# Performance work log

Hardware: AMD Instinct MI355X
Metric: run time of the kernel (lower is better)

The kernel has to match this reference:

```python
import jax, jax.numpy as jnp
import numpy as np

N_SLOTS = 65536
KEY_DIM = 64
VAL_DIM = 64
N_QUERIES = 8192
TOPK = 4
LR = 1e-3
MOMENTUM = 0.9
WD = 1e-4


def setup_inputs() -> dict:
    key = jax.random.key(0)
    k1, k2, k3, k4 = jax.random.split(key, 4)
    return {
        "queries": jax.random.normal(k1, (N_QUERIES, KEY_DIM), jnp.float32),
        "grads": jax.random.normal(k2, (N_QUERIES, TOPK, VAL_DIM), jnp.float32) * 0.05,
        "keys": jax.random.normal(k3, (N_SLOTS, KEY_DIM), jnp.float32) * 0.02,
        "vals": jax.random.normal(k4, (N_SLOTS, VAL_DIM), jnp.float32) * 0.02,
        "mom_vals": jnp.zeros((N_SLOTS, VAL_DIM), jnp.float32),
        "topk": TOPK,
    }


def reference(queries, grads, keys, vals, mom_vals, topk):
    # --- retrieve_topk ---
    sim = queries @ keys.T                      # [N, n_slots]
    _, idx = jax.lax.top_k(sim, topk)           # [N, topk] int32
    retrieved = vals[idx]                       # [N, topk, val_dim]

    # --- inner_update (no_grad in original) ---
    n_slots, val_dim = vals.shape
    idx_flat = idx.reshape(-1)                  # [N*topk]
    grads_flat = grads.reshape(-1, val_dim)     # [N*topk, val_dim]
    slot_grads = jax.ops.segment_sum(grads_flat, idx_flat, num_segments=n_slots)
    counts = jax.ops.segment_sum(
        jnp.ones_like(idx_flat, dtype=jnp.float32), idx_flat, num_segments=n_slots
    )
    mask = counts > 0
    # average grads per touched slot; untouched slots stay zero
    slot_grads = jnp.where(mask[:, None], slot_grads / jnp.maximum(counts, 1.0)[:, None], slot_grads)

    new_mom = MOMENTUM * mom_vals + slot_grads
    update_delta = -LR * (new_mom + WD * vals)
    final_update = jnp.where(mask[:, None], update_delta, 0.0)
    new_vals = vals + final_update
    return retrieved, idx, new_vals, new_mom
```

## Files before the change

kernel.cpp:

```cpp
#include <hip/hip_runtime.h>
#include <stdint.h>

#define N_SLOTS   65536
#define KEY_DIM   64
#define VAL_DIM   64
#define N_QUERIES 8192
#define TOPK      4
#define LR        1e-3f
#define MOMENTUM  0.9f
#define WD        1e-4f

#define NCHUNK 16
#define CHUNK  (N_SLOTS / NCHUNK)
#define TILE_SLOTS 128
#define TILES_PER_CHUNK (CHUNK / TILE_SLOTS)
#define SUBT 8
#define QPB 128

#define ZF4   ((N_SLOTS * VAL_DIM + N_SLOTS) / 4)
#define ZBLK  (ZF4 / 256)
#define QBLK  (N_QUERIES * 8 / 256)
#define KBLK  (N_SLOTS * 8 / 256)

typedef __attribute__((ext_vector_type(8))) _Float16 f16x8;
typedef __attribute__((ext_vector_type(2))) __fp16   fp16x2;
typedef __attribute__((ext_vector_type(4))) float    f32x4;
union F16 { uint4 u; f16x8 h; };
union PK  { fp16x2 h2; uint32_t u; };

__device__ __forceinline__ uint32_t pk2(float a, float b) {
    PK p; p.h2 = __builtin_amdgcn_cvt_pkrtz(a, b); return p.u;
}

__device__ __forceinline__ uint32_t med3u(uint32_t a, uint32_t b, uint32_t c) {
    uint32_t d;
    asm("v_med3_u32 %0, %1, %2, %3" : "=v"(d) : "v"(a), "v"(b), "v"(c));
    return d;
}

__device__ __forceinline__ uint64_t ord64(double d) {
    uint64_t u = (uint64_t)__double_as_longlong(d);
    return (u & 0x8000000000000000ull) ? ~u : (u | 0x8000000000000000ull);
}
__device__ __forceinline__ void ins4(uint64_t* t, uint64_t key) {
    if (key > t[3]) {
        t[3] = key;
        if (t[3] > t[2]) { uint64_t x = t[2]; t[2] = t[3]; t[3] = x; }
        if (t[2] > t[1]) { uint64_t x = t[1]; t[1] = t[2]; t[2] = x; }
        if (t[1] > t[0]) { uint64_t x = t[0]; t[0] = t[1]; t[1] = x; }
    }
}
__device__ __forceinline__ void cswap64(uint64_t& x, uint64_t& y) {
    uint64_t hi = x > y ? x : y;
    uint64_t lo = x > y ? y : x;
    x = hi; y = lo;
}
__device__ __forceinline__ void merge4_64(uint64_t* a, uint64_t b0, uint64_t b1,
                                          uint64_t b2, uint64_t b3) {
    uint64_t m0 = a[0] > b3 ? a[0] : b3;
    uint64_t m1 = a[1] > b2 ? a[1] : b2;
    uint64_t m2 = a[2] > b1 ? a[2] : b1;
    uint64_t m3 = a[3] > b0 ? a[3] : b0;
    cswap64(m0, m2); cswap64(m1, m3); cswap64(m0, m1); cswap64(m2, m3);
    a[0] = m0; a[1] = m1; a[2] = m2; a[3] = m3;
}
__device__ __forceinline__ void cswap32(uint32_t& x, uint32_t& y) {
    uint32_t hi = max(x, y);
    uint32_t lo = min(x, y);
    x = hi; y = lo;
}
__device__ __forceinline__ void merge4_32(uint32_t* a, uint32_t b0, uint32_t b1,
                                          uint32_t b2, uint32_t b3) {
    uint32_t m0 = max(a[0], b3);
    uint32_t m1 = max(a[1], b2);
    uint32_t m2 = max(a[2], b1);
    uint32_t m3 = max(a[3], b0);
    cswap32(m0, m2); cswap32(m1, m3); cswap32(m0, m1); cswap32(m2, m3);
    a[0] = m0; a[1] = m1; a[2] = m2; a[3] = m3;
}

__device__ __forceinline__ void gload16(const void* g, void* l) {
    __builtin_amdgcn_global_load_lds(
        (const __attribute__((address_space(1))) uint32_t*)g,
        (__attribute__((address_space(3))) uint32_t*)l, 16, 0, 0);
}

__global__ void kA_pack(const float* __restrict__ queries,
                        const float* __restrict__ keys,
                        uint4* __restrict__ qpack, uint4* __restrict__ kpack,
                        float4* __restrict__ zbuf) {
    const int b = blockIdx.x, tid = threadIdx.x;
    if (b < ZBLK) {
        zbuf[b * 256 + tid] = (float4){0.f, 0.f, 0.f, 0.f};
    } else if (b < ZBLK + QBLK) {
        int e = (b - ZBLK) * 256 + tid;
        const float4* src = (const float4*)(queries + (size_t)e * 8);
        float4 a = src[0], v = src[1];
        uint4 u;
        u.x = pk2(a.x, a.y); u.y = pk2(a.z, a.w);
        u.z = pk2(v.x, v.y); u.w = pk2(v.z, v.w);
        qpack[e] = u;
    } else {
        int e = (b - ZBLK - QBLK) * 256 + tid;
        int slot = e >> 3, k8 = e & 7;
        const float4* src = (const float4*)(keys + (size_t)slot * KEY_DIM + k8 * 8);
        float4 a = src[0], v = src[1];
        uint4 u;
        u.x = pk2(a.x, a.y); u.y = pk2(a.z, a.w);
        u.z = pk2(v.x, v.y); u.w = pk2(v.z, v.w);
        int tile = slot >> 7, r = slot & 127;
        kpack[(size_t)tile * 1024 + r * 8 + (k8 ^ (r & 7))] = u;
    }
}

__global__ __launch_bounds__(256, 4) void k1_screen(
        const uint4* __restrict__ qpack, const uint4* __restrict__ kpack,
        uint32_t* __restrict__ cand) {
    __shared__ uint4 sbuf[2048];

    const int tid = threadIdx.x;
    const int w = tid >> 6, lane = tid & 63;
    const int lcol = lane & 15, lrow = lane >> 4;
    const int chunk  = blockIdx.x;
    const int qblock = blockIdx.y;

    f16x8 B[2][2];
    #pragma unroll
    for (int j = 0; j < 2; ++j) {
        #pragma unroll
        for (int ks = 0; ks < 2; ++ks) {
            int q = qblock * QPB + w * 32 + j * 16 + lcol;
            F16 t; t.u = qpack[q * 8 + lrow + ks * 4];
            B[j][ks] = t.h;
        }
    }

    uint32_t kk[2][4] = {{0u,0u,0u,0u},{0u,0u,0u,0u}};

    const uint4* gbase = kpack + (size_t)(chunk * TILES_PER_CHUNK) * 1024;
    const int x0 = lrow ^ (lcol & 7);
    const int base_b = lcol * 128 + x0 * 16;
    const f32x4 zacc = {4.0f, 4.0f, 4.0f, 4.0f};

#define STAGE(tt, bb) do {                                                    \
        const uint4* gg = gbase + (size_t)(tt) * 1024 + w * 256 + lane;       \
        char* ldst = (char*)sbuf + (bb) * 16384 + w * 4096;                   \
        _Pragma("unroll")                                                     \
        for (int i_ = 0; i_ < 4; ++i_)                                        \
            gload16((const void*)(gg + i_ * 64), (void*)(ldst + i_ * 1024));  \
    } while (0)

    STAGE(0, 0);

    #pragma unroll 1
    for (int t = 0; t < TILES_PER_CHUNK; ++t) {
        __syncthreads();
        if (t < TILES_PER_CHUNK - 1) STAGE(t + 1, (t + 1) & 1);
        const char* sbb = (const char*)sbuf + (t & 1) * 16384;
        const uint32_t tbase = (uint32_t)(t * 32) + (uint32_t)lrow;

        #pragma unroll
        for (int sub = 0; sub < SUBT; ++sub) {
            uint4 ua0 = *(const uint4*)(sbb + base_b + sub * 2048);
            uint4 ua1 = *(const uint4*)(sbb + (base_b ^ 64) + sub * 2048);
            F16 a0, a1; a0.u = ua0; a1.u = ua1;
            const uint32_t idb = tbase + (uint32_t)(sub * 4);

            #pragma unroll
            for (int j = 0; j < 2; ++j) {
                f32x4 acc = __builtin_amdgcn_mfma_f32_16x16x32_f16(a0.h, B[j][0], zacc, 0, 0, 0);
                acc = __builtin_amdgcn_mfma_f32_16x16x32_f16(a1.h, B[j][1], acc, 0, 0, 0);
                float m = fmaxf(fmaxf(fmaxf(acc[0], acc[1]), acc[2]), acc[3]);
                uint32_t key = (__float_as_uint(m) & 0xFFFFFC00u) | idb;
                uint32_t t0 = kk[j][0], t1 = kk[j][1], t2 = kk[j][2], t3 = kk[j][3];
                kk[j][0] = max(t0, key);
                kk[j][1] = med3u(t0, t1, key);
                kk[j][2] = med3u(t1, t2, key);
                kk[j][3] = med3u(t2, t3, key);
            }
        }
    }
#undef STAGE

    #pragma unroll
    for (int j = 0; j < 2; ++j) {
        uint32_t s4[4] = {kk[j][0], kk[j][1], kk[j][2], kk[j][3]};
        #pragma unroll
        for (int m = 16; m <= 32; m <<= 1) {
            uint32_t b0 = (uint32_t)__shfl_xor((int)s4[0], m, 64);
            uint32_t b1 = (uint32_t)__shfl_xor((int)s4[1], m, 64);
            uint32_t b2 = (uint32_t)__shfl_xor((int)s4[2], m, 64);
            uint32_t b3 = (uint32_t)__shfl_xor((int)s4[3], m, 64);
            merge4_32(s4, b0, b1, b2, b3);
        }
        if (lane < 16) {
            int q = qblock * QPB + w * 32 + j * 16 + lane;
            uint4 c;
            c.x = s4[0] & 1023u; c.y = s4[1] & 1023u;
            c.z = s4[2] & 1023u; c.w = s4[3] & 1023u;
            *(uint4*)&cand[((size_t)q * NCHUNK + chunk) * 4] = c;
        }
    }
}

__global__ __launch_bounds__(256) void k2_rescore(
        const uint32_t* __restrict__ cand,
        const float* __restrict__ queries, const float* __restrict__ keys,
        const float* __restrict__ vals, const float* __restrict__ grads,
        float* __restrict__ retrieved, float* __restrict__ idx_f,
        float* __restrict__ slot_grads, float* __restrict__ counts) {
    int w = threadIdx.x >> 6, lane = threadIdx.x & 63;
    int q = blockIdx.x * 4 + w;
    int seg = lane & 3;

    const float4* qp = (const float4*)(queries + (size_t)q * KEY_DIM);
    float4 q0 = qp[seg * 4 + 0], q1 = qp[seg * 4 + 1];
    float4 q2 = qp[seg * 4 + 2], q3 = qp[seg * 4 + 3];
    const uint32_t* cq = cand + (size_t)q * 64;

    uint64_t s4[4] = {0ull, 0ull, 0ull, 0ull};
    #pragma unroll 4
    for (int it = 0; it < 16; ++it) {
        int r = it * 16 + (lane >> 2);
        uint32_t grow = cq[r >> 2];
        int slot = (r >> 4) * CHUNK + (int)(grow >> 2) * 16
                 + (int)(grow & 3) * 4 + (r & 3);
        const float4* kp = (const float4*)(keys + (size_t)slot * KEY_DIM) + seg * 4;
        float4 k0 = kp[0], k1 = kp[1], k2 = kp[2], k3 = kp[3];
        double ac0 = 0.0, ac1 = 0.0;
        ac0 = fma((double)q0.x, (double)k0.x, ac0);
        ac1 = fma((double)q0.y, (double)k0.y, ac1);
        ac0 = fma((double)q0.z, (double)k0.z, ac0);
        ac1 = fma((double)q0.w, (double)k0.w, ac1);
        ac0 = fma((double)q1.x, (double)k1.x, ac0);
        ac1 = fma((double)q1.y, (double)k1.y, ac1);
        ac0 = fma((double)q1.z, (double)k1.z, ac0);
        ac1 = fma((double)q1.w, (double)k1.w, ac1);
        ac0 = fma((double)q2.x, (double)k2.x, ac0);
        ac1 = fma((double)q2.y, (double)k2.y, ac1);
        ac0 = fma((double)q2.z, (double)k2.z, ac0);
        ac1 = fma((double)q2.w, (double)k2.w, ac1);
        ac0 = fma((double)q3.x, (double)k3.x, ac0);
        ac1 = fma((double)q3.y, (double)k3.y, ac1);
        ac0 = fma((double)q3.z, (double)k3.z, ac0);
        ac1 = fma((double)q3.w, (double)k3.w, ac1);
        double acc = ac0 + ac1;
        acc += __shfl_xor(acc, 1, 64);
        acc += __shfl_xor(acc, 2, 64);
        uint64_t key = (ord64(acc) & 0xFFFFFFFFFFFF0000ull)
                     | (uint64_t)((~(uint32_t)slot) & 0xFFFFu);
        if (seg != 0) key = 0ull;
        ins4(s4, key);
    }
    #pragma unroll
    for (int m = 1; m <= 32; m <<= 1) {
        uint64_t b0 = (uint64_t)__shfl_xor((unsigned long long)s4[0], m, 64);
        uint64_t b1 = (uint64_t)__shfl_xor((unsigned long long)s4[1], m, 64);
        uint64_t b2 = (uint64_t)__shfl_xor((unsigned long long)s4[2], m, 64);
        uint64_t b3 = (uint64_t)__shfl_xor((unsigned long long)s4[3], m, 64);
        merge4_64(s4, b0, b1, b2, b3);
    }
    int sl0 = (int)((~(uint32_t)s4[0]) & 0xFFFFu);
    int sl1 = (int)((~(uint32_t)s4[1]) & 0xFFFFu);
    int sl2 = (int)((~(uint32_t)s4[2]) & 0xFFFFu);
    int sl3 = (int)((~(uint32_t)s4[3]) & 0xFFFFu);
    if (lane == 0) {
        idx_f[q * TOPK + 0] = (float)sl0;
        idx_f[q * TOPK + 1] = (float)sl1;
        idx_f[q * TOPK + 2] = (float)sl2;
        idx_f[q * TOPK + 3] = (float)sl3;
    }
    int slots[4] = {sl0, sl1, sl2, sl3};
    #pragma unroll
    for (int r = 0; r < 4; ++r) {
        int s = slots[r];
        float g = grads[(size_t)q * 256 + r * 64 + lane];
        retrieved[(size_t)q * 256 + r * 64 + lane] = vals[(size_t)s * 64 + lane];
        atomicAdd(&slot_grads[(size_t)s * 64 + lane], g);
        if (lane == 0) atomicAdd(&counts[s], 1.0f);
    }
}

__global__ void k4_update(const float* __restrict__ vals,
                          const float* __restrict__ mom,
                          const float* __restrict__ slot_grads,
                          const float* __restrict__ counts,
                          float* __restrict__ new_vals,
                          float* __restrict__ new_mom) {
    int e4 = blockIdx.x * 256 + threadIdx.x;
    int slot = e4 >> 4;
    float c = counts[slot];
    float4 g  = ((const float4*)slot_grads)[e4];
    float4 mv = ((const float4*)mom)[e4];
    float4 v  = ((const float4*)vals)[e4];
    float inv = 1.0f / fmaxf(c, 1.0f);
    float sel = (c > 0.0f) ? -LR : 0.0f;
    float4 nm, nv;
    nm.x = MOMENTUM * mv.x + g.x * inv;  nv.x = v.x + sel * (nm.x + WD * v.x);
    nm.y = MOMENTUM * mv.y + g.y * inv;  nv.y = v.y + sel * (nm.y + WD * v.y);
    nm.z = MOMENTUM * mv.z + g.z * inv;  nv.z = v.z + sel * (nm.z + WD * v.z);
    nm.w = MOMENTUM * mv.w + g.w * inv;  nv.w = v.w + sel * (nm.w + WD * v.w);
    ((float4*)new_vals)[e4] = nv;
    ((float4*)new_mom)[e4]  = nm;
}

extern "C" void kernel_launch(void* const* d_in, const int* in_sizes, int n_in,
                              void* d_out, int out_size, void* d_ws, size_t ws_size,
                              hipStream_t stream) {
    const float* queries = (const float*)d_in[0];
    const float* grads   = (const float*)d_in[1];
    const float* keys    = (const float*)d_in[2];
    const float* vals    = (const float*)d_in[3];
    const float* mom     = (const float*)d_in[4];

    float* out = (float*)d_out;
    float* retrieved = out;
    float* idx_f     = retrieved + (size_t)N_QUERIES * TOPK * VAL_DIM;
    float* new_vals  = idx_f + (size_t)N_QUERIES * TOPK;
    float* new_mom   = new_vals + (size_t)N_SLOTS * VAL_DIM;

    float*    slot_grads = (float*)d_ws;
    float*    counts     = slot_grads + (size_t)N_SLOTS * VAL_DIM;
    uint4*    qpack = (uint4*)(counts + N_SLOTS);
    uint4*    kpack = qpack + (size_t)N_QUERIES * 8;
    uint32_t* cand  = (uint32_t*)(kpack + (size_t)(N_SLOTS / TILE_SLOTS) * 1024);

    hipLaunchKernelGGL(kA_pack, dim3(ZBLK + QBLK + KBLK), dim3(256), 0, stream,
                       queries, keys, qpack, kpack, (float4*)slot_grads);
    hipLaunchKernelGGL(k1_screen, dim3(NCHUNK, N_QUERIES / QPB), dim3(256), 0, stream,
                       qpack, kpack, cand);
    hipLaunchKernelGGL(k2_rescore, dim3(N_QUERIES / 4), dim3(256), 0, stream,
                       cand, queries, keys, vals, grads,
                       retrieved, idx_f, slot_grads, counts);
    hipLaunchKernelGGL(k4_update, dim3(N_SLOTS * VAL_DIM / 4 / 256), dim3(256),
                       0, stream, vals, mom, slot_grads, counts, new_vals, new_mom);
}
```

Before: 153.2 us.

## Halve screening chunks and queries per block, one query group per wave

The coarse screening pass now uses 8 slot chunks instead of 16 and 64 queries per block instead of 128, so each wave handles one 16-query group instead of two. The candidate index field widens to 11 bits, and the rescoring kernel gathers half as many candidates (32 per query). This lowers rescoring gather work and candidate storage. The cost is fewer MFMAs per LDS tile load and coarser candidate pruning (top-4 per 2048-slot chunk), which could hurt recall and screening efficiency.

New measurement: 156.6 us. 1.02x slower.

```diff
diff --git a/kernel.cpp b/kernel.cpp
--- a/kernel.cpp
+++ b/kernel.cpp
@@ -10,12 +10,12 @@
 #define MOMENTUM  0.9f
 #define WD        1e-4f
 
-#define NCHUNK 16
+#define NCHUNK 8
 #define CHUNK  (N_SLOTS / NCHUNK)
 #define TILE_SLOTS 128
 #define TILES_PER_CHUNK (CHUNK / TILE_SLOTS)
 #define SUBT 8
-#define QPB 128
+#define QPB 64
 
 #define ZF4   ((N_SLOTS * VAL_DIM + N_SLOTS) / 4)
 #define ZBLK  (ZF4 / 256)
@@ -124,18 +124,15 @@
     const int chunk  = blockIdx.x;
     const int qblock = blockIdx.y;
 
-    f16x8 B[2][2];
+    f16x8 B[2];
     #pragma unroll
-    for (int j = 0; j < 2; ++j) {
-        #pragma unroll
-        for (int ks = 0; ks < 2; ++ks) {
-            int q = qblock * QPB + w * 32 + j * 16 + lcol;
-            F16 t; t.u = qpack[q * 8 + lrow + ks * 4];
-            B[j][ks] = t.h;
-        }
-    }
-
-    uint32_t kk[2][4] = {{0u,0u,0u,0u},{0u,0u,0u,0u}};
+    for (int ks = 0; ks < 2; ++ks) {
+        int q = qblock * QPB + w * 16 + lcol;
+        F16 t; t.u = qpack[q * 8 + lrow + ks * 4];
+        B[ks] = t.h;
+    }
+
+    uint32_t kk[4] = {0u, 0u, 0u, 0u};
 
     const uint4* gbase = kpack + (size_t)(chunk * TILES_PER_CHUNK) * 1024;
     const int x0 = lrow ^ (lcol & 7);
@@ -166,25 +163,21 @@
             F16 a0, a1; a0.u = ua0; a1.u = ua1;
             const uint32_t idb = tbase + (uint32_t)(sub * 4);
 
-            #pragma unroll
-            for (int j = 0; j < 2; ++j) {
-                f32x4 acc = __builtin_amdgcn_mfma_f32_16x16x32_f16(a0.h, B[j][0], zacc, 0, 0, 0);
-                acc = __builtin_amdgcn_mfma_f32_16x16x32_f16(a1.h, B[j][1], acc, 0, 0, 0);
-                float m = fmaxf(fmaxf(fmaxf(acc[0], acc[1]), acc[2]), acc[3]);
-                uint32_t key = (__float_as_uint(m) & 0xFFFFFC00u) | idb;
-                uint32_t t0 = kk[j][0], t1 = kk[j][1], t2 = kk[j][2], t3 = kk[j][3];
-                kk[j][0] = max(t0, key);
-                kk[j][1] = med3u(t0, t1, key);
-                kk[j][2] = med3u(t1, t2, key);
-                kk[j][3] = med3u(t2, t3, key);
-            }
+            f32x4 acc = __builtin_amdgcn_mfma_f32_16x16x32_f16(a0.h, B[0], zacc, 0, 0, 0);
+            acc = __builtin_amdgcn_mfma_f32_16x16x32_f16(a1.h, B[1], acc, 0, 0, 0);
+            float m = fmaxf(fmaxf(fmaxf(acc[0], acc[1]), acc[2]), acc[3]);
+            uint32_t key = (__float_as_uint(m) & 0xFFFFF800u) | idb;
+            uint32_t t0 = kk[0], t1 = kk[1], t2 = kk[2], t3 = kk[3];
+            kk[0] = max(t0, key);
+            kk[1] = med3u(t0, t1, key);
+            kk[2] = med3u(t1, t2, key);
+            kk[3] = med3u(t2, t3, key);
         }
     }
 #undef STAGE
 
-    #pragma unroll
-    for (int j = 0; j < 2; ++j) {
-        uint32_t s4[4] = {kk[j][0], kk[j][1], kk[j][2], kk[j][3]};
+    {
+        uint32_t s4[4] = {kk[0], kk[1], kk[2], kk[3]};
         #pragma unroll
         for (int m = 16; m <= 32; m <<= 1) {
             uint32_t b0 = (uint32_t)__shfl_xor((int)s4[0], m, 64);
@@ -194,10 +187,10 @@
             merge4_32(s4, b0, b1, b2, b3);
         }
         if (lane < 16) {
-            int q = qblock * QPB + w * 32 + j * 16 + lane;
+            int q = qblock * QPB + w * 16 + lane;
             uint4 c;
-            c.x = s4[0] & 1023u; c.y = s4[1] & 1023u;
-            c.z = s4[2] & 1023u; c.w = s4[3] & 1023u;
+            c.x = s4[0] & 2047u; c.y = s4[1] & 2047u;
+            c.z = s4[2] & 2047u; c.w = s4[3] & 2047u;
             *(uint4*)&cand[((size_t)q * NCHUNK + chunk) * 4] = c;
         }
     }
@@ -216,11 +209,11 @@
     const float4* qp = (const float4*)(queries + (size_t)q * KEY_DIM);
     float4 q0 = qp[seg * 4 + 0], q1 = qp[seg * 4 + 1];
     float4 q2 = qp[seg * 4 + 2], q3 = qp[seg * 4 + 3];
-    const uint32_t* cq = cand + (size_t)q * 64;
+    const uint32_t* cq = cand + (size_t)q * 32;
 
     uint64_t s4[4] = {0ull, 0ull, 0ull, 0ull};
     #pragma unroll 4
-    for (int it = 0; it < 16; ++it) {
+    for (int it = 0; it < 8; ++it) {
         int r = it * 16 + (lane >> 2);
         uint32_t grow = cq[r >> 2];
         int slot = (r >> 4) * CHUNK + (int)(grow >> 2) * 16
```

## Prefilter rescore candidates to top-8 groups using approximate scores before fp64 rescoring

Applied to the files above, without the earlier changes.

The candidate kernel now stores full approximate scores alongside group indices. The rescore kernel uses them to select the best 8 of 64 candidate groups per query with two butterfly top-4 passes, then rescores only those 32 slots in fp64. Each dot product is split across 2 lanes instead of 4. This cuts the rescore's key loads and fp64 FMAs to about an eighth, but if the approximate scores misrank a true top-4 slot outside the kept groups, results can differ.

Result: faster. 126.1 us (-17.7%).

```diff
diff --git a/kernel.cpp b/kernel.cpp
--- a/kernel.cpp
+++ b/kernel.cpp
@@ -42,14 +42,6 @@
     uint64_t u = (uint64_t)__double_as_longlong(d);
     return (u & 0x8000000000000000ull) ? ~u : (u | 0x8000000000000000ull);
 }
-__device__ __forceinline__ void ins4(uint64_t* t, uint64_t key) {
-    if (key > t[3]) {
-        t[3] = key;
-        if (t[3] > t[2]) { uint64_t x = t[2]; t[2] = t[3]; t[3] = x; }
-        if (t[2] > t[1]) { uint64_t x = t[1]; t[1] = t[2]; t[2] = x; }
-        if (t[1] > t[0]) { uint64_t x = t[0]; t[0] = t[1]; t[1] = x; }
-    }
-}
 __device__ __forceinline__ void cswap64(uint64_t& x, uint64_t& y) {
     uint64_t hi = x > y ? x : y;
     uint64_t lo = x > y ? y : x;
@@ -78,6 +70,16 @@
     cswap32(m0, m2); cswap32(m1, m3); cswap32(m0, m1); cswap32(m2, m3);
     a[0] = m0; a[1] = m1; a[2] = m2; a[3] = m3;
 }
+
+#define BFLY64(S)                                                             \
+    _Pragma("unroll")                                                         \
+    for (int m_ = 1; m_ <= 32; m_ <<= 1) {                                    \
+        uint64_t b0_ = (uint64_t)__shfl_xor((unsigned long long)S[0], m_, 64);\
+        uint64_t b1_ = (uint64_t)__shfl_xor((unsigned long long)S[1], m_, 64);\
+        uint64_t b2_ = (uint64_t)__shfl_xor((unsigned long long)S[2], m_, 64);\
+        uint64_t b3_ = (uint64_t)__shfl_xor((unsigned long long)S[3], m_, 64);\
+        merge4_64(S, b0_, b1_, b2_, b3_);                                     \
+    }
 
 __device__ __forceinline__ void gload16(const void* g, void* l) {
     __builtin_amdgcn_global_load_lds(
@@ -196,8 +198,7 @@
         if (lane < 16) {
             int q = qblock * QPB + w * 32 + j * 16 + lane;
             uint4 c;
-            c.x = s4[0] & 1023u; c.y = s4[1] & 1023u;
-            c.z = s4[2] & 1023u; c.w = s4[3] & 1023u;
+            c.x = s4[0]; c.y = s4[1]; c.z = s4[2]; c.w = s4[3];
             *(uint4*)&cand[((size_t)q * NCHUNK + chunk) * 4] = c;
         }
     }
@@ -211,59 +212,50 @@
         float* __restrict__ slot_grads, float* __restrict__ counts) {
     int w = threadIdx.x >> 6, lane = threadIdx.x & 63;
     int q = blockIdx.x * 4 + w;
-    int seg = lane & 3;
-
-    const float4* qp = (const float4*)(queries + (size_t)q * KEY_DIM);
-    float4 q0 = qp[seg * 4 + 0], q1 = qp[seg * 4 + 1];
-    float4 q2 = qp[seg * 4 + 2], q3 = qp[seg * 4 + 3];
-    const uint32_t* cq = cand + (size_t)q * 64;
-
-    uint64_t s4[4] = {0ull, 0ull, 0ull, 0ull};
-    #pragma unroll 4
-    for (int it = 0; it < 16; ++it) {
-        int r = it * 16 + (lane >> 2);
-        uint32_t grow = cq[r >> 2];
-        int slot = (r >> 4) * CHUNK + (int)(grow >> 2) * 16
-                 + (int)(grow & 3) * 4 + (r & 3);
-        const float4* kp = (const float4*)(keys + (size_t)slot * KEY_DIM) + seg * 4;
-        float4 k0 = kp[0], k1 = kp[1], k2 = kp[2], k3 = kp[3];
-        double ac0 = 0.0, ac1 = 0.0;
-        ac0 = fma((double)q0.x, (double)k0.x, ac0);
-        ac1 = fma((double)q0.y, (double)k0.y, ac1);
-        ac0 = fma((double)q0.z, (double)k0.z, ac0);
-        ac1 = fma((double)q0.w, (double)k0.w, ac1);
-        ac0 = fma((double)q1.x, (double)k1.x, ac0);
-        ac1 = fma((double)q1.y, (double)k1.y, ac1);
-        ac0 = fma((double)q1.z, (double)k1.z, ac0);
-        ac1 = fma((double)q1.w, (double)k1.w, ac1);
-        ac0 = fma((double)q2.x, (double)k2.x, ac0);
-        ac1 = fma((double)q2.y, (double)k2.y, ac1);
-        ac0 = fma((double)q2.z, (double)k2.z, ac0);
-        ac1 = fma((double)q2.w, (double)k2.w, ac1);
-        ac0 = fma((double)q3.x, (double)k3.x, ac0);
-        ac1 = fma((double)q3.y, (double)k3.y, ac1);
-        ac0 = fma((double)q3.z, (double)k3.z, ac0);
-        ac1 = fma((double)q3.w, (double)k3.w, ac1);
-        double acc = ac0 + ac1;
-        acc += __shfl_xor(acc, 1, 64);
-        acc += __shfl_xor(acc, 2, 64);
-        uint64_t key = (ord64(acc) & 0xFFFFFFFFFFFF0000ull)
-                     | (uint64_t)((~(uint32_t)slot) & 0xFFFFu);
-        if (seg != 0) key = 0ull;
-        ins4(s4, key);
-    }
+
+    uint32_t key32 = cand[(size_t)q * 64 + lane];
+    uint64_t aug = ((uint64_t)key32 << 14)
+                 | (uint64_t)((uint32_t)(lane >> 2) << 10)
+                 | (uint64_t)(key32 & 1023u);
+    uint64_t s4[4] = {aug, 0ull, 0ull, 0ull};
+    BFLY64(s4);
+    uint64_t aug2 = (aug == s4[0] || aug == s4[1] ||
+                     aug == s4[2] || aug == s4[3]) ? 0ull : aug;
+    uint64_t r4[4] = {aug2, 0ull, 0ull, 0ull};
+    BFLY64(r4);
+
+    int r = lane >> 1, seg = lane & 1;
+    int g = r >> 2, rr = r & 3;
+    uint64_t tg = g == 0 ? s4[0] : g == 1 ? s4[1] : g == 2 ? s4[2] : g == 3 ? s4[3]
+                : g == 4 ? r4[0] : g == 5 ? r4[1] : g == 6 ? r4[2] : r4[3];
+    uint32_t low = (uint32_t)tg & 0x3FFFu;
+    int chn = (int)(low >> 10);
+    int id  = (int)(low & 1023u);
+    int slot = chn * CHUNK + (id >> 2) * 16 + (id & 3) * 4 + rr;
+
+    const float4* qp = (const float4*)(queries + (size_t)q * KEY_DIM) + seg * 8;
+    const float4* kp = (const float4*)(keys + (size_t)slot * KEY_DIM) + seg * 8;
+    double ac0 = 0.0, ac1 = 0.0;
     #pragma unroll
-    for (int m = 1; m <= 32; m <<= 1) {
-        uint64_t b0 = (uint64_t)__shfl_xor((unsigned long long)s4[0], m, 64);
-        uint64_t b1 = (uint64_t)__shfl_xor((unsigned long long)s4[1], m, 64);
-        uint64_t b2 = (uint64_t)__shfl_xor((unsigned long long)s4[2], m, 64);
-        uint64_t b3 = (uint64_t)__shfl_xor((unsigned long long)s4[3], m, 64);
-        merge4_64(s4, b0, b1, b2, b3);
-    }
-    int sl0 = (int)((~(uint32_t)s4[0]) & 0xFFFFu);
-    int sl1 = (int)((~(uint32_t)s4[1]) & 0xFFFFu);
-    int sl2 = (int)((~(uint32_t)s4[2]) & 0xFFFFu);
-    int sl3 = (int)((~(uint32_t)s4[3]) & 0xFFFFu);
+    for (int u = 0; u < 8; ++u) {
+        float4 qv = qp[u], kv = kp[u];
+        ac0 = fma((double)qv.x, (double)kv.x, ac0);
+        ac1 = fma((double)qv.y, (double)kv.y, ac1);
+        ac0 = fma((double)qv.z, (double)kv.z, ac0);
+        ac1 = fma((double)qv.w, (double)kv.w, ac1);
+    }
+    double acc = ac0 + ac1;
+    acc += __shfl_xor(acc, 1, 64);
+    uint64_t fkey = (ord64(acc) & 0xFFFFFFFFFFFF0000ull)
+                  | (uint64_t)((~(uint32_t)slot) & 0xFFFFu);
+    if (seg != 0) fkey = 0ull;
+    uint64_t f4[4] = {fkey, 0ull, 0ull, 0ull};
+    BFLY64(f4);
+
+    int sl0 = (int)((~(uint32_t)f4[0]) & 0xFFFFu);
+    int sl1 = (int)((~(uint32_t)f4[1]) & 0xFFFFu);
+    int sl2 = (int)((~(uint32_t)f4[2]) & 0xFFFFu);
+    int sl3 = (int)((~(uint32_t)f4[3]) & 0xFFFFu);
     if (lane == 0) {
         idx_f[q * TOPK + 0] = (float)sl0;
         idx_f[q * TOPK + 1] = (float)sl1;
@@ -272,11 +264,11 @@
     }
     int slots[4] = {sl0, sl1, sl2, sl3};
     #pragma unroll
-    for (int r = 0; r < 4; ++r) {
-        int s = slots[r];
-        float g = grads[(size_t)q * 256 + r * 64 + lane];
-        retrieved[(size_t)q * 256 + r * 64 + lane] = vals[(size_t)s * 64 + lane];
-        atomicAdd(&slot_grads[(size_t)s * 64 + lane], g);
+    for (int rr2 = 0; rr2 < 4; ++rr2) {
+        int s = slots[rr2];
+        float gg = grads[(size_t)q * 256 + rr2 * 64 + lane];
+        retrieved[(size_t)q * 256 + rr2 * 64 + lane] = vals[(size_t)s * 64 + lane];
+        atomicAdd(&slot_grads[(size_t)s * 64 + lane], gg);
         if (lane == 0) atomicAdd(&counts[s], 1.0f);
     }
 }
```
